# Kernel tuning notes

Hardware: AMD Instinct MI355X
Metric: run time of the kernel (lower is better)

## Reference

```python
import jax, jax.numpy as jnp
import numpy as np

EPS = 1e-5


def conv2d(x, w, b=None, stride=1, padding=0, dilation=1, groups=1):
    out = jax.lax.conv_general_dilated(
        x, w, (stride, stride), [(padding, padding), (padding, padding)],
        rhs_dilation=(dilation, dilation),
        dimension_numbers=('NCHW', 'OIHW', 'NCHW'),
        feature_group_count=groups)
    if b is not None:
        out = out + b[None, :, None, None]
    return out


def unfold3(x):
    # torch nn.Unfold(kernel=3, padding=1), kept as [b, c, 9, h, w]
    # (channel-major ordering c*9+k, k = row-major kernel index, matches torch)
    b, c, h, w = x.shape
    xp = jnp.pad(x, ((0, 0), (0, 0), (1, 1), (1, 1)))
    return jnp.stack([xp[:, :, i:i + h, j:j + w]
                      for i in range(3) for j in range(3)], axis=2)


def setup_inputs():
    B, C, O, H, W = 8, 64, 64, 128, 128
    key = jax.random.key(0)
    ks = jax.random.split(key, 16)
    s = 0.05
    rn = lambda k, shape: jax.random.normal(k, shape, jnp.float32) * s
    return {
        'x': jax.random.normal(ks[0], (B, C, H, W), jnp.float32),
        'cdcm_conv1_w': rn(ks[1], (C, C, 1, 1)),
        'cdcm_conv1_b': jnp.zeros((C,), jnp.float32),
        'cdcm_w5': rn(ks[2], (C, C, 3, 3)),
        'cdcm_w7': rn(ks[3], (C, C, 3, 3)),
        'cdcm_w9': rn(ks[4], (C, C, 3, 3)),
        'cdcm_w11': rn(ks[5], (C, C, 3, 3)),
        'dsc_dw_w': rn(ks[6], (C, 1, 3, 3)),
        'dsc_dw_b': jnp.zeros((C,), jnp.float32),
        'dsc_pw_w': rn(ks[7], (C, C, 1, 1)),
        'dsc_pw_b': jnp.zeros((C,), jnp.float32),
        'gw_w': rn(ks[8], (C, 9, 9)),
        'gw_b': jnp.zeros((C, 9), jnp.float32),
        'gw_bn_g': jnp.ones((C, 9), jnp.float32),
        'gw_bn_b': jnp.zeros((C, 9), jnp.float32),
        'gw_bn_m': jnp.zeros((C, 9), jnp.float32),
        'gw_bn_v': jnp.ones((C, 9), jnp.float32),
        'conv_w': rn(ks[9], (O, C, 3, 3)),
        'conv_b': jnp.zeros((O,), jnp.float32),
        'fr_w': rn(ks[10], (O, O, 1, 1)),
        'fr_b': jnp.zeros((O,), jnp.float32),
        'ens_w': rn(ks[11], (3, O, O, 3, 3)),
        'ens_b': jnp.zeros((3, O), jnp.float32),
        'bn_g': jnp.ones((O,), jnp.float32),
        'bn_b': jnp.zeros((O,), jnp.float32),
        'bn_m': jnp.zeros((O,), jnp.float32),
        'bn_v': jnp.ones((O,), jnp.float32),
    }


def reference(x, cdcm_conv1_w, cdcm_conv1_b, cdcm_w5, cdcm_w7, cdcm_w9, cdcm_w11,
              dsc_dw_w, dsc_dw_b, dsc_pw_w, dsc_pw_b,
              gw_w, gw_b, gw_bn_g, gw_bn_b, gw_bn_m, gw_bn_v,
              conv_w, conv_b, fr_w, fr_b, ens_w, ens_b,
              bn_g, bn_b, bn_m, bn_v):
    C = x.shape[1]
    # ---- CDCM: relu -> 1x1 conv -> 4 dilated 3x3 convs, each through the
    # SAME DepthwiseSeparableConv instance, then summed ----
    y = conv2d(jax.nn.relu(x), cdcm_conv1_w, cdcm_conv1_b)

    def dsc(z):
        z = conv2d(z, dsc_dw_w, dsc_dw_b, padding=1, groups=C)
        return conv2d(z, dsc_pw_w, dsc_pw_b)

    y = sum(dsc(conv2d(y, w, padding=d, dilation=d))
            for w, d in ((cdcm_w5, 5), (cdcm_w7, 7), (cdcm_w9, 9), (cdcm_w11, 11)))

    b, c, h, w = y.shape
    patches = unfold3(y)  # [b, c, 9, h, w]

    # ---- dynamic weight generation: grouped 1x1 conv (groups=c, 9->9 per
    # group) + inference BatchNorm over the c*9 channels + softmax over the 9
    # patch positions ----
    gw = jnp.einsum('coi,bcihw->bcohw', gw_w, patches) + gw_b[None, :, :, None, None]
    scale = (gw_bn_g / jnp.sqrt(gw_bn_v + EPS))[None, :, :, None, None]
    gw = (gw - gw_bn_m[None, :, :, None, None]) * scale + gw_bn_b[None, :, :, None, None]
    wsm = jax.nn.softmax(gw, axis=2)

    # ---- involution core: the rearrange to (3h,3w) + stride-3 3x3 conv is
    # exactly a contraction of (patches * weights) with the conv kernel over
    # the 9 kernel positions (row-major kernel index == patch index) ----
    prod = patches * wsm  # [b, c, 9, h, w]
    O = conv_w.shape[0]
    out = jnp.einsum('bckhw,ock->bohw', prod, conv_w.reshape(O, c, 9)) + conv_b[None, :, None, None]

    # ---- feature reuse: conv1x1(conv_out) + conv_out ----
    out = conv2d(out, fr_w, fr_b) + out

    # ---- ensemble: mean of 3 conv3x3 ----
    out = jnp.mean(jnp.stack([conv2d(out, ens_w[i], ens_b[i], padding=1)
                              for i in range(3)]), axis=0)

    # ---- final BN (inference) + ReLU ----
    out = (out - bn_m[None, :, None, None]) * (bn_g / jnp.sqrt(bn_v + EPS))[None, :, None, None] \
          + bn_b[None, :, None, None]
    return jax.nn.relu(out)
```

## Files before the change

### kernel.cpp

```cpp
#include <hip/hip_runtime.h>
#include <hip/hip_bf16.h>
#include <hip/hip_fp16.h>

#define EPSV 1e-5f
#define Bn 8
#define Cn 64
#define Hn 128
#define Wn 128
#define Pn (Hn*Wn)
#define PR 150
#define PE 130
#define YPAD_ELEMS (Bn*PR*PR*Cn)

typedef _Float16 v8h __attribute__((ext_vector_type(8)));
typedef float v16f __attribute__((ext_vector_type(16)));
typedef unsigned short ushort8v __attribute__((ext_vector_type(8)));
typedef unsigned short ushort4v __attribute__((ext_vector_type(4)));

__device__ __forceinline__ unsigned short f2h(float v) {
  _Float16 h = (_Float16)v;
  return *reinterpret_cast<const unsigned short*>(&h);
}

__device__ __forceinline__ v8h exp8h(v8h x) {
  union { v8h v; __half2 h[4]; } u; u.v = x;
  #pragma unroll
  for (int i = 0; i < 4; i++) u.h[i] = h2exp(u.h[i]);
  return u.v;
}
__device__ __forceinline__ v8h rcp8h(v8h x) {
  union { v8h v; __half2 h[4]; } u; u.v = x;
  #pragma unroll
  for (int i = 0; i < 4; i++) u.h[i] = h2rcp(u.h[i]);
  return u.v;
}

__device__ __forceinline__ size_t clb(int b, int row, int kb, int col, int PD) {
  return ((((size_t)b * PD + row) * 4 + kb) * PD + col) * 16;
}

__device__ __forceinline__ void swz_bh(int& b, int& h) {
  int bid = blockIdx.x;
  int w = (bid & 7) * 128 + (bid >> 3);
  b = w >> 7; h = w & 127;
}

__global__ __launch_bounds__(256) void k_prep(
    const float* __restrict__ w1, const float* __restrict__ w5,
    const float* __restrict__ w7, const float* __restrict__ w9,
    const float* __restrict__ w11, const float* __restrict__ pww,
    const float* __restrict__ frw, const float* __restrict__ cw,
    const float* __restrict__ gww, const float* __restrict__ gwb,
    const float* __restrict__ gbg, const float* __restrict__ gbb,
    const float* __restrict__ gbm, const float* __restrict__ gbv,
    const float* __restrict__ ensw, const float* __restrict__ ensb,
    const float* __restrict__ bng, const float* __restrict__ bnb,
    const float* __restrict__ bnm, const float* __restrict__ bnv,
    unsigned short* __restrict__ apack, unsigned short* __restrict__ apinv,
    unsigned short* __restrict__ apens, unsigned short* __restrict__ appw1,
    unsigned short* __restrict__ appw, unsigned short* __restrict__ apfr,
    unsigned short* __restrict__ apid, unsigned short* __restrict__ gwpk,
    unsigned short* __restrict__ apk, unsigned short* __restrict__ bpk,
    float* __restrict__ esc, float* __restrict__ ebi)
{
  int id = blockIdx.x * 256 + threadIdx.x;
  if (id < 147456) {
    int e = id & 7, l = (id >> 3) & 63, mh = (id >> 9) & 1,
        kb = (id >> 10) & 3, tap = id >> 12;
    int d = tap / 9, k9 = tap - 9 * d;
    int m = mh * 32 + (l & 31);
    int c = kb * 16 + (l >> 5) * 8 + e;
    const float* src = (d == 0) ? w5 : (d == 1) ? w7 : (d == 2) ? w9 : w11;
    apack[id] = f2h(src[(m * 64 + c) * 9 + k9]);
    return;
  }
  id -= 147456;
  if (id < 36864) {
    int e = id & 7, l = (id >> 3) & 63, mh = (id >> 9) & 1,
        kb = (id >> 10) & 3, tap = id >> 12;
    int m = mh * 32 + (l & 31);
    int c = kb * 16 + (l >> 5) * 8 + e;
    apinv[id] = f2h(cw[(m * 64 + c) * 9 + tap]);
    return;
  }
  id -= 36864;
  if (id < 36864) {
    int e = id & 7, l = (id >> 3) & 63, mh = (id >> 9) & 1,
        kb = (id >> 10) & 3, tap = id >> 12;
    int m = mh * 32 + (l & 31);
    int c = kb * 16 + (l >> 5) * 8 + e;
    float v = (ensw[((0 * 64 + m) * 64 + c) * 9 + tap] +
               ensw[((64 + m) * 64 + c) * 9 + tap] +
               ensw[((128 + m) * 64 + c) * 9 + tap]) * (1.f / 3.f);
    apens[id] = f2h(v);
    return;
  }
  id -= 36864;
  if (id < 4096) {
    int e = id & 7, l = (id >> 3) & 63, mh = (id >> 9) & 1, kb = (id >> 10) & 3;
    int m = mh * 32 + (l & 31);
    int c = kb * 16 + (l >> 5) * 8 + e;
    appw1[id] = f2h(w1[m * 64 + c]);
    return;
  }
  id -= 4096;
  if (id < 4096) {
    int e = id & 7, l = (id >> 3) & 63, mh = (id >> 9) & 1, kb = (id >> 10) & 3;
    int m = mh * 32 + (l & 31);
    int c = kb * 16 + (l >> 5) * 8 + e;
    appw[id] = f2h(pww[m * 64 + c]);
    return;
  }
  id -= 4096;
  if (id < 4096) {
    int e = id & 7, l = (id >> 3) & 63, mh = (id >> 9) & 1, kb = (id >> 10) & 3;
    int m = mh * 32 + (l & 31);
    int c = kb * 16 + (l >> 5) * 8 + e;
    apfr[id] = f2h(frw[m * 64 + c]);
    return;
  }
  id -= 4096;
  if (id < 4096) {
    int e = id & 7, l = (id >> 3) & 63, mh = (id >> 9) & 1, kb = (id >> 10) & 3;
    int m = mh * 32 + (l & 31);
    int c = kb * 16 + (l >> 5) * 8 + e;
    apid[id] = f2h((m == c) ? 1.f : 0.f);
    return;
  }
  id -= 4096;
  if (id < 5184) {
    int cblk = id / 648, r = id - cblk * 648;
    int tap = r >> 3, ch = r & 7;
    int c = cblk * 8 + ch;
    gwpk[id] = f2h(gww[c * 81 + tap]);
    return;
  }
  id -= 5184;
  if (id < 576) {
    int cblk = id / 72, r = id - cblk * 72;
    int o = r >> 3, ch = r & 7;
    int c = cblk * 8 + ch;
    float A = gbg[c * 9 + o] / sqrtf(gbv[c * 9 + o] + EPSV);
    apk[id] = f2h(A);
    return;
  }
  id -= 576;
  if (id < 576) {
    int cblk = id / 72, r = id - cblk * 72;
    int o = r >> 3, ch = r & 7;
    int c = cblk * 8 + ch;
    float A = gbg[c * 9 + o] / sqrtf(gbv[c * 9 + o] + EPSV);
    float B = (gwb[c * 9 + o] - gbm[c * 9 + o]) * A + gbb[c * 9 + o];
    bpk[id] = f2h(B);
    return;
  }
  id -= 576;
  if (id < 64) {
    float s = bng[id] / sqrtf(bnv[id] + EPSV);
    esc[id] = s;
    float bm = (ensb[id] + ensb[64 + id] + ensb[128 + id]) * (1.f / 3.f);
    ebi[id] = (bm - bnm[id]) * s + bnb[id];
  }
}

__global__ __launch_bounds__(256) void k_zb(unsigned short* __restrict__ buf,
                                            int PD, int pad)
{
  int per_b = 2 * pad * PD + 128 * 2 * pad;
  int id = blockIdx.x * 256 + threadIdx.x;
  int b = id / per_b;
  if (b >= Bn) return;
  int r = id - b * per_b;
  int tb = 2 * pad * PD;
  int row, col;
  if (r < tb) {
    int rr = r / PD; col = r - rr * PD;
    row = (rr < pad) ? rr : (rr + 128);
  } else {
    int r2 = r - tb;
    row = pad + r2 / (2 * pad);
    int cc = r2 - (r2 / (2 * pad)) * (2 * pad);
    col = (cc < pad) ? cc : (cc + 128);
  }
  ushort8v z = {0, 0, 0, 0, 0, 0, 0, 0};
  #pragma unroll
  for (int kb = 0; kb < 4; kb++) {
    unsigned short* p = buf + clb(b, row, kb, col, PD);
    *(ushort8v*)p = z;
    *(ushort8v*)(p + 8) = z;
  }
}

__global__ __launch_bounds__(256, 4) void k_pw1x(const float* __restrict__ x,
    const unsigned short* __restrict__ apw, const float* __restrict__ bias,
    unsigned short* __restrict__ ypad)
{
  int b, h; swz_bh(b, h);
  const int tid = threadIdx.x, wv = tid >> 6, l = tid & 63;
  const int ln31 = l & 31, g = l >> 5;
  const int px = wv * 32 + ln31;
  const float* xb = x + ((size_t)b * Cn) * Pn + h * Wn + px;
  v16f acc0, acc1;
  #pragma unroll
  for (int r = 0; r < 16; r++) { acc0[r] = 0.f; acc1[r] = 0.f; }
  const unsigned short* apl = apw + l * 8;
  #pragma unroll
  for (int kb = 0; kb < 4; kb++) {
    int c0 = kb * 16 + g * 8;
    v8h Bf;
    #pragma unroll
    for (int e = 0; e < 8; e++)
      Bf[e] = (_Float16)fmaxf(xb[(size_t)(c0 + e) * Pn], 0.f);
    v8h A0 = *(const v8h*)(apl + (kb * 2) * 512);
    v8h A1 = *(const v8h*)(apl + (kb * 2 + 1) * 512);
    acc0 = __builtin_amdgcn_mfma_f32_32x32x16_f16(A0, Bf, acc0, 0, 0, 0);
    acc1 = __builtin_amdgcn_mfma_f32_32x32x16_f16(A1, Bf, acc1, 0, 0, 0);
  }
  #pragma unroll
  for (int t = 0; t < 4; t++) {
    int c0 = 8 * t + 4 * g;
    int kb = c0 >> 4, sub = c0 & 15;
    ushort4v s0, s1;
    #pragma unroll
    for (int u = 0; u < 4; u++) {
      s0[u] = f2h(acc0[4 * t + u] + bias[c0 + u]);
      s1[u] = f2h(acc1[4 * t + u] + bias[c0 + u + 32]);
    }
    *(ushort4v*)(ypad + clb(b, h + 11, kb, px + 11, PR) + sub) = s0;
    *(ushort4v*)(ypad + clb(b, h + 11, kb + 2, px + 11, PR) + sub) = s1;
  }
}

__global__ __launch_bounds__(256) void k_cdcm_mfma(
    const unsigned short* __restrict__ ypad,
    const unsigned short* __restrict__ apack,
    unsigned short* __restrict__ spad)
{
  __shared__ __align__(16) unsigned short Abuf[36864];
  int b, h; swz_bh(b, h);
  const int tid = threadIdx.x, wv = tid >> 6, l = tid & 63;
  const int ln31 = l & 31, g = l >> 5;

  v16f acc0, acc1;
  #pragma unroll
  for (int r = 0; r < 16; r++) { acc0[r] = 0.f; acc1[r] = 0.f; }

  const unsigned short* abl = Abuf + l * 8;

  for (int d = 0; d < 4; d++) {
    __syncthreads();
    {
      const ushort8v* src = (const ushort8v*)(apack + d * 36864);
      ushort8v* dst = (ushort8v*)Abuf;
      #pragma unroll
      for (int it = 0; it < 18; it++)
        dst[tid + it * 256] = src[tid + it * 256];
    }
    __syncthreads();

    const int dil = 5 + 2 * d;
    #pragma unroll
    for (int ky = 0; ky < 3; ky++) {
      const int row = h + 11 + (ky - 1) * dil;
      #pragma unroll
      for (int kx = 0; kx < 3; kx++) {
        const int col = wv * 32 + ln31 + (kx - 1) * dil + 11;
        const int t9 = ky * 3 + kx;
        const unsigned short* ap = abl + t9 * 4096;
        #pragma unroll
        for (int kb = 0; kb < 4; kb++) {
          v8h Bf = *(const v8h*)(ypad + clb(b, row, kb, col, PR) + g * 8);
          v8h A0 = *(const v8h*)(ap + kb * 1024);
          v8h A1 = *(const v8h*)(ap + kb * 1024 + 512);
          acc0 = __builtin_amdgcn_mfma_f32_32x32x16_f16(A0, Bf, acc0, 0, 0, 0);
          acc1 = __builtin_amdgcn_mfma_f32_32x32x16_f16(A1, Bf, acc1, 0, 0, 0);
        }
      }
    }
  }
  const int px = wv * 32 + ln31;
  #pragma unroll
  for (int t = 0; t < 4; t++) {
    int c0 = 8 * t + 4 * g;
    int kb = c0 >> 4, sub = c0 & 15;
    ushort4v s0, s1;
    #pragma unroll
    for (int u = 0; u < 4; u++) {
      s0[u] = f2h(acc0[4 * t + u]);
      s1[u] = f2h(acc1[4 * t + u]);
    }
    *(ushort4v*)(spad + clb(b, h + 1, kb, px + 1, PE) + sub) = s0;
    *(ushort4v*)(spad + clb(b, h + 1, kb + 2, px + 1, PE) + sub) = s1;
  }
}

__global__ __launch_bounds__(256, 4) void k_dwpw_mfma(
    const unsigned short* __restrict__ spad,
    const float* __restrict__ dww, const float* __restrict__ dwb,
    const unsigned short* __restrict__ appw, const float* __restrict__ pwb,
    unsigned short* __restrict__ y2pad)
{
  __shared__ float wdw[576];
  __shared__ float bdw[64];
  const int tid = threadIdx.x;
  for (int t = tid; t < 576; t += 256) wdw[t] = dww[t];
  if (tid < 64) bdw[tid] = dwb[tid];
  __syncthreads();

  int b, h; swz_bh(b, h);
  const int wv = tid >> 6, l = tid & 63;
  const int ln31 = l & 31, g = l >> 5;
  const int w = wv * 32 + ln31;

  v16f acc0, acc1;
  #pragma unroll
  for (int r = 0; r < 16; r++) { acc0[r] = 0.f; acc1[r] = 0.f; }
  const unsigned short* apl = appw + l * 8;

  #pragma unroll
  for (int kb = 0; kb < 4; kb++) {
    const int c0 = kb * 16 + g * 8;
    v8h t[9];
    #pragma unroll
    for (int k = 0; k < 9; k++) {
      const int dy = k / 3 - 1, dx = k % 3 - 1;
      t[k] = *(const v8h*)(spad + clb(b, h + 1 + dy, kb, w + 1 + dx, PE) + g * 8);
    }
    v8h dvh;
    #pragma unroll
    for (int e = 0; e < 8; e++) {
      const int c = c0 + e;
      float a = 4.f * bdw[c];
      #pragma unroll
      for (int k = 0; k < 9; k++) a += wdw[c * 9 + k] * (float)t[k][e];
      dvh[e] = (_Float16)a;
    }
    v8h A0 = *(const v8h*)(apl + (kb * 2) * 512);
    v8h A1 = *(const v8h*)(apl + (kb * 2 + 1) * 512);
    acc0 = __builtin_amdgcn_mfma_f32_32x32x16_f16(A0, dvh, acc0, 0, 0, 0);
    acc1 = __builtin_amdgcn_mfma_f32_32x32x16_f16(A1, dvh, acc1, 0, 0, 0);
  }
  #pragma unroll
  for (int t = 0; t < 4; t++) {
    int c0 = 8 * t + 4 * g;
    int kb = c0 >> 4, sub = c0 & 15;
    ushort4v s0, s1;
    #pragma unroll
    for (int u = 0; u < 4; u++) {
      s0[u] = f2h(acc0[4 * t + u] + 4.f * pwb[c0 + u]);
      s1[u] = f2h(acc1[4 * t + u] + 4.f * pwb[c0 + u + 32]);
    }
    *(ushort4v*)(y2pad + clb(b, h + 1, kb, w + 1, PE) + sub) = s0;
    *(ushort4v*)(y2pad + clb(b, h + 1, kb + 2, w + 1, PE) + sub) = s1;
  }
}

__global__ __launch_bounds__(256, 3) void k_invol_mfma(
    const unsigned short* __restrict__ y2pad,
    const unsigned short* __restrict__ gwpk,
    const unsigned short* __restrict__ apk,
    const unsigned short* __restrict__ bpk,
    const unsigned short* __restrict__ apinv,
    const float* __restrict__ cbias,
    unsigned short* __restrict__ ipad)
{
  __shared__ __align__(16) unsigned short gws[5184];
  __shared__ __align__(16) unsigned short As[576];
  __shared__ __align__(16) unsigned short Bs[576];
  const int tid = threadIdx.x;
  for (int t = tid; t < 648; t += 256)
    ((ushort8v*)gws)[t] = ((const ushort8v*)gwpk)[t];
  if (tid < 72) {
    ((ushort8v*)As)[tid] = ((const ushort8v*)apk)[tid];
    ((ushort8v*)Bs)[tid] = ((const ushort8v*)bpk)[tid];
  }
  __syncthreads();

  int b, h; swz_bh(b, h);
  const int wv = tid >> 6, l = tid & 63;
  const int p32 = l & 31, g = l >> 5;
  const int w = wv * 32 + p32;

  v16f acc0, acc1;
  #pragma unroll
  for (int r = 0; r < 16; r++) { acc0[r] = 0.f; acc1[r] = 0.f; }

  for (int cb4 = 0; cb4 < 4; cb4++) {
    const int cblk = cb4 * 2 + g;
    const unsigned short* gwp = gws + cblk * 648;
    const unsigned short* Ap = As + cblk * 72;
    const unsigned short* Bp = Bs + cblk * 72;

    v8h pt[9];
    #pragma unroll
    for (int k = 0; k < 9; k++) {
      const int dy = k / 3 - 1, dx = k % 3 - 1;
      pt[k] = *(const v8h*)(y2pad + clb(b, h + 1 + dy, cb4, w + 1 + dx, PE) + g * 8);
    }
    v8h s[9];
    #pragma unroll
    for (int o = 0; o < 9; o++) {
      v8h a = (*(const v8h*)(gwp + o * 72)) * pt[0];
      #pragma unroll
      for (int i = 1; i < 9; i++)
        a += (*(const v8h*)(gwp + o * 72 + i * 8)) * pt[i];
      s[o] = a * (*(const v8h*)(Ap + o * 8)) + (*(const v8h*)(Bp + o * 8));
    }
    v8h esum = {0, 0, 0, 0, 0, 0, 0, 0};
    #pragma unroll
    for (int o = 0; o < 9; o++) { s[o] = exp8h(s[o]); esum += s[o]; }
    v8h inv = rcp8h(esum);
    #pragma unroll
    for (int k = 0; k < 9; k++) pt[k] = pt[k] * s[k] * inv;

    const unsigned short* ap = apinv + l * 8;
    #pragma unroll
    for (int k = 0; k < 9; k++) {
      const unsigned short* a2 = ap + ((k * 4 + cb4) * 2) * 512;
      v8h A0 = *(const v8h*)(a2);
      v8h A1 = *(const v8h*)(a2 + 512);
      acc0 = __builtin_amdgcn_mfma_f32_32x32x16_f16(A0, pt[k], acc0, 0, 0, 0);
      acc1 = __builtin_amdgcn_mfma_f32_32x32x16_f16(A1, pt[k], acc1, 0, 0, 0);
    }
  }
  #pragma unroll
  for (int t = 0; t < 4; t++) {
    int c0 = 8 * t + 4 * g;
    int kb = c0 >> 4, sub = c0 & 15;
    ushort4v s0, s1;
    #pragma unroll
    for (int u = 0; u < 4; u++) {
      s0[u] = f2h(acc0[4 * t + u] + cbias[c0 + u]);
      s1[u] = f2h(acc1[4 * t + u] + cbias[c0 + u + 32]);
    }
    *(ushort4v*)(ipad + clb(b, h, kb, w, 128) + sub) = s0;
    *(ushort4v*)(ipad + clb(b, h, kb + 2, w, 128) + sub) = s1;
  }
}

__global__ __launch_bounds__(256, 4) void k_fr_mfma(
    const unsigned short* __restrict__ ipad,
    const unsigned short* __restrict__ apfr,
    const unsigned short* __restrict__ apid,
    const float* __restrict__ bias,
    unsigned short* __restrict__ opad)
{
  int b, h; swz_bh(b, h);
  const int tid = threadIdx.x, wv = tid >> 6, l = tid & 63;
  const int ln31 = l & 31, g = l >> 5;
  const int px = wv * 32 + ln31;
  v16f acc0, acc1;
  #pragma unroll
  for (int r = 0; r < 16; r++) { acc0[r] = 0.f; acc1[r] = 0.f; }
  const unsigned short* apl = apfr + l * 8;
  const unsigned short* idl = apid + l * 8;
  #pragma unroll
  for (int kb = 0; kb < 4; kb++) {
    v8h Bf = *(const v8h*)(ipad + clb(b, h, kb, px, 128) + g * 8);
    v8h A0 = *(const v8h*)(apl + (kb * 2) * 512);
    v8h A1 = *(const v8h*)(apl + (kb * 2 + 1) * 512);
    v8h I0 = *(const v8h*)(idl + (kb * 2) * 512);
    v8h I1 = *(const v8h*)(idl + (kb * 2 + 1) * 512);
    acc0 = __builtin_amdgcn_mfma_f32_32x32x16_f16(A0, Bf, acc0, 0, 0, 0);
    acc1 = __builtin_amdgcn_mfma_f32_32x32x16_f16(A1, Bf, acc1, 0, 0, 0);
    acc0 = __builtin_amdgcn_mfma_f32_32x32x16_f16(I0, Bf, acc0, 0, 0, 0);
    acc1 = __builtin_amdgcn_mfma_f32_32x32x16_f16(I1, Bf, acc1, 0, 0, 0);
  }
  #pragma unroll
  for (int t = 0; t < 4; t++) {
    int c0 = 8 * t + 4 * g;
    int kb = c0 >> 4, sub = c0 & 15;
    ushort4v s0, s1;
    #pragma unroll
    for (int u = 0; u < 4; u++) {
      s0[u] = f2h(acc0[4 * t + u] + bias[c0 + u]);
      s1[u] = f2h(acc1[4 * t + u] + bias[c0 + u + 32]);
    }
    *(ushort4v*)(opad + clb(b, h + 1, kb, px + 1, PE) + sub) = s0;
    *(ushort4v*)(opad + clb(b, h + 1, kb + 2, px + 1, PE) + sub) = s1;
  }
}

__global__ __launch_bounds__(256) void k_ens_mfma(
    const unsigned short* __restrict__ opad,
    const unsigned short* __restrict__ apens,
    const float* __restrict__ esc, const float* __restrict__ ebi,
    float* __restrict__ out)
{
  __shared__ __align__(16) unsigned short Abuf[36864];
  const int tid = threadIdx.x;
  {
    const ushort8v* src = (const ushort8v*)apens;
    ushort8v* dst = (ushort8v*)Abuf;
    #pragma unroll
    for (int it = 0; it < 18; it++)
      dst[tid + it * 256] = src[tid + it * 256];
  }
  __syncthreads();

  int b, h; swz_bh(b, h);
  const int wv = tid >> 6, l = tid & 63;
  const int ln31 = l & 31, g = l >> 5;

  v16f acc0, acc1;
  #pragma unroll
  for (int r = 0; r < 16; r++) { acc0[r] = 0.f; acc1[r] = 0.f; }

  const unsigned short* abl = Abuf + l * 8;

  #pragma unroll
  for (int ky = 0; ky < 3; ky++) {
    #pragma unroll
    for (int kx = 0; kx < 3; kx++) {
      const int tap = ky * 3 + kx;
      const int row = h + ky;
      const int col = wv * 32 + ln31 + kx;
      const unsigned short* ap = abl + tap * 4096;
      #pragma unroll
      for (int kb = 0; kb < 4; kb++) {
        v8h Bf = *(const v8h*)(opad + clb(b, row, kb, col, PE) + g * 8);
        v8h A0 = *(const v8h*)(ap + kb * 1024);
        v8h A1 = *(const v8h*)(ap + kb * 1024 + 512);
        acc0 = __builtin_amdgcn_mfma_f32_32x32x16_f16(A0, Bf, acc0, 0, 0, 0);
        acc1 = __builtin_amdgcn_mfma_f32_32x32x16_f16(A1, Bf, acc1, 0, 0, 0);
      }
    }
  }
  float* sp = out + ((size_t)b * Cn) * Pn + h * Wn + wv * 32 + ln31;
  #pragma unroll
  for (int r = 0; r < 16; r++) {
    int o0 = (r & 3) + 8 * (r >> 2) + 4 * g;
    float v0 = acc0[r] * esc[o0] + ebi[o0];
    float v1 = acc1[r] * esc[o0 + 32] + ebi[o0 + 32];
    sp[(size_t)o0 * Pn] = fmaxf(v0, 0.f);
    sp[(size_t)(o0 + 32) * Pn] = fmaxf(v1, 0.f);
  }
}

extern "C" void kernel_launch(void* const* d_in, const int* in_sizes, int n_in,
                              void* d_out, int out_size, void* d_ws, size_t ws_size,
                              hipStream_t stream)
{
  const float* x    = (const float*)d_in[0];
  const float* w1   = (const float*)d_in[1];
  const float* b1   = (const float*)d_in[2];
  const float* w5   = (const float*)d_in[3];
  const float* w7   = (const float*)d_in[4];
  const float* w9   = (const float*)d_in[5];
  const float* w11  = (const float*)d_in[6];
  const float* dww  = (const float*)d_in[7];
  const float* dwb  = (const float*)d_in[8];
  const float* pww  = (const float*)d_in[9];
  const float* pwb  = (const float*)d_in[10];
  const float* gww  = (const float*)d_in[11];
  const float* gwb  = (const float*)d_in[12];
  const float* gbg  = (const float*)d_in[13];
  const float* gbb  = (const float*)d_in[14];
  const float* gbm  = (const float*)d_in[15];
  const float* gbv  = (const float*)d_in[16];
  const float* cw   = (const float*)d_in[17];
  const float* cb   = (const float*)d_in[18];
  const float* frw  = (const float*)d_in[19];
  const float* frb  = (const float*)d_in[20];
  const float* ensw = (const float*)d_in[21];
  const float* ensb = (const float*)d_in[22];
  const float* bng  = (const float*)d_in[23];
  const float* bnb  = (const float*)d_in[24];
  const float* bnm  = (const float*)d_in[25];
  const float* bnv  = (const float*)d_in[26];

  unsigned short* wsu   = (unsigned short*)d_ws;
  unsigned short* ypad  = wsu;
  unsigned short* y2pad = wsu;
  unsigned short* opad  = wsu;
  unsigned short* apack = wsu + YPAD_ELEMS;
  unsigned short* apinv = apack + 147456;
  unsigned short* apens = apinv + 36864;
  unsigned short* appw1 = apens + 36864;
  unsigned short* appw  = appw1 + 4096;
  unsigned short* apfr  = appw + 4096;
  unsigned short* apid  = apfr + 4096;
  unsigned short* gwpk  = apid + 4096;
  unsigned short* apk   = gwpk + 5184;
  unsigned short* bpk   = apk + 576;
  float* esc = (float*)(bpk + 576);
  float* ebi = esc + 64;

  unsigned short* spad = (unsigned short*)d_out;
  unsigned short* ipad = (unsigned short*)d_out;
  float* D = (float*)d_out;

  k_prep<<<953, 256, 0, stream>>>(w1, w5, w7, w9, w11, pww, frw, cw,
                                  gww, gwb, gbg, gbb, gbm, gbv, ensw, ensb,
                                  bng, bnb, bnm, bnv,
                                  apack, apinv, apens, appw1, appw, apfr, apid,
                                  gwpk, apk, bpk, esc, ebi);
  k_zb<<<192, 256, 0, stream>>>(ypad, PR, 11);
  k_zb<<<17, 256, 0, stream>>>(spad, PE, 1);

  k_pw1x<<<1024, 256, 0, stream>>>(x, appw1, b1, ypad);
  k_cdcm_mfma<<<1024, 256, 0, stream>>>(ypad, apack, spad);
  k_zb<<<17, 256, 0, stream>>>(y2pad, PE, 1);
  k_dwpw_mfma<<<1024, 256, 0, stream>>>(spad, dww, dwb, appw, pwb, y2pad);
  k_invol_mfma<<<1024, 256, 0, stream>>>(y2pad, gwpk, apk, bpk, apinv, cb, ipad);
  k_fr_mfma<<<1024, 256, 0, stream>>>(ipad, apfr, apid, frb, opad);
  k_ens_mfma<<<1024, 256, 0, stream>>>(opad, apens, esc, ebi, D);
}
```

Before: 166.5 us.

## Compute two output rows per block in dilated and ensemble convs; drop identity MFMA

The CDCM and ensemble conv kernels now give each block two output rows, with four accumulators. Each LDS-staged A fragment is reused across both rows and the grid is halved, which cuts the LDS weight reload per row. The feature-reuse kernel stops adding the residual through an identity-matrix MFMA and instead reads the fp16 input and adds it in the epilogue, so the identity weight pack is removed. The costs are higher register pressure from four v16f accumulators, fewer blocks, and the loss of the block-to-(b,h) swizzle.

```diff
diff --git a/kernel.cpp b/kernel.cpp
--- a/kernel.cpp
+++ b/kernel.cpp
@@ -20,6 +20,9 @@
 __device__ __forceinline__ unsigned short f2h(float v) {
   _Float16 h = (_Float16)v;
   return *reinterpret_cast<const unsigned short*>(&h);
+}
+__device__ __forceinline__ float h2f(unsigned short u) {
+  return (float)(*reinterpret_cast<const _Float16*>(&u));
 }
 
 __device__ __forceinline__ v8h exp8h(v8h x) {
@@ -59,7 +62,7 @@
     unsigned short* __restrict__ apack, unsigned short* __restrict__ apinv,
     unsigned short* __restrict__ apens, unsigned short* __restrict__ appw1,
     unsigned short* __restrict__ appw, unsigned short* __restrict__ apfr,
-    unsigned short* __restrict__ apid, unsigned short* __restrict__ gwpk,
+    unsigned short* __restrict__ gwpk,
     unsigned short* __restrict__ apk, unsigned short* __restrict__ bpk,
     float* __restrict__ esc, float* __restrict__ ebi)
 {
@@ -117,14 +120,6 @@
     int m = mh * 32 + (l & 31);
     int c = kb * 16 + (l >> 5) * 8 + e;
     apfr[id] = f2h(frw[m * 64 + c]);
-    return;
-  }
-  id -= 4096;
-  if (id < 4096) {
-    int e = id & 7, l = (id >> 3) & 63, mh = (id >> 9) & 1, kb = (id >> 10) & 3;
-    int m = mh * 32 + (l & 31);
-    int c = kb * 16 + (l >> 5) * 8 + e;
-    apid[id] = f2h((m == c) ? 1.f : 0.f);
     return;
   }
   id -= 4096;
@@ -237,13 +232,14 @@
     unsigned short* __restrict__ spad)
 {
   __shared__ __align__(16) unsigned short Abuf[36864];
-  int b, h; swz_bh(b, h);
+  const int bid = blockIdx.x;
+  const int b = bid & 7, h0 = (bid >> 3) * 2;
   const int tid = threadIdx.x, wv = tid >> 6, l = tid & 63;
   const int ln31 = l & 31, g = l >> 5;
 
-  v16f acc0, acc1;
-  #pragma unroll
-  for (int r = 0; r < 16; r++) { acc0[r] = 0.f; acc1[r] = 0.f; }
+  v16f a00, a01, a10, a11;
+  #pragma unroll
+  for (int r = 0; r < 16; r++) { a00[r] = 0.f; a01[r] = 0.f; a10[r] = 0.f; a11[r] = 0.f; }
 
   const unsigned short* abl = Abuf + l * 8;
 
@@ -261,7 +257,7 @@
     const int dil = 5 + 2 * d;
     #pragma unroll
     for (int ky = 0; ky < 3; ky++) {
-      const int row = h + 11 + (ky - 1) * dil;
+      const int r0 = h0 + 11 + (ky - 1) * dil;
       #pragma unroll
       for (int kx = 0; kx < 3; kx++) {
         const int col = wv * 32 + ln31 + (kx - 1) * dil + 11;
@@ -269,11 +265,14 @@
         const unsigned short* ap = abl + t9 * 4096;
         #pragma unroll
         for (int kb = 0; kb < 4; kb++) {
-          v8h Bf = *(const v8h*)(ypad + clb(b, row, kb, col, PR) + g * 8);
+          v8h B0 = *(const v8h*)(ypad + clb(b, r0, kb, col, PR) + g * 8);
+          v8h B1 = *(const v8h*)(ypad + clb(b, r0 + 1, kb, col, PR) + g * 8);
           v8h A0 = *(const v8h*)(ap + kb * 1024);
           v8h A1 = *(const v8h*)(ap + kb * 1024 + 512);
-          acc0 = __builtin_amdgcn_mfma_f32_32x32x16_f16(A0, Bf, acc0, 0, 0, 0);
-          acc1 = __builtin_amdgcn_mfma_f32_32x32x16_f16(A1, Bf, acc1, 0, 0, 0);
+          a00 = __builtin_amdgcn_mfma_f32_32x32x16_f16(A0, B0, a00, 0, 0, 0);
+          a01 = __builtin_amdgcn_mfma_f32_32x32x16_f16(A1, B0, a01, 0, 0, 0);
+          a10 = __builtin_amdgcn_mfma_f32_32x32x16_f16(A0, B1, a10, 0, 0, 0);
+          a11 = __builtin_amdgcn_mfma_f32_32x32x16_f16(A1, B1, a11, 0, 0, 0);
         }
       }
     }
@@ -283,14 +282,18 @@
   for (int t = 0; t < 4; t++) {
     int c0 = 8 * t + 4 * g;
     int kb = c0 >> 4, sub = c0 & 15;
-    ushort4v s0, s1;
+    ushort4v s0, s1, s2, s3;
     #pragma unroll
     for (int u = 0; u < 4; u++) {
-      s0[u] = f2h(acc0[4 * t + u]);
-      s1[u] = f2h(acc1[4 * t + u]);
-    }
-    *(ushort4v*)(spad + clb(b, h + 1, kb, px + 1, PE) + sub) = s0;
-    *(ushort4v*)(spad + clb(b, h + 1, kb + 2, px + 1, PE) + sub) = s1;
+      s0[u] = f2h(a00[4 * t + u]);
+      s1[u] = f2h(a01[4 * t + u]);
+      s2[u] = f2h(a10[4 * t + u]);
+      s3[u] = f2h(a11[4 * t + u]);
+    }
+    *(ushort4v*)(spad + clb(b, h0 + 1, kb, px + 1, PE) + sub) = s0;
+    *(ushort4v*)(spad + clb(b, h0 + 1, kb + 2, px + 1, PE) + sub) = s1;
+    *(ushort4v*)(spad + clb(b, h0 + 2, kb, px + 1, PE) + sub) = s2;
+    *(ushort4v*)(spad + clb(b, h0 + 2, kb + 2, px + 1, PE) + sub) = s3;
   }
 }
 
@@ -441,7 +444,6 @@
 __global__ __launch_bounds__(256, 4) void k_fr_mfma(
     const unsigned short* __restrict__ ipad,
     const unsigned short* __restrict__ apfr,
-    const unsigned short* __restrict__ apid,
     const float* __restrict__ bias,
     unsigned short* __restrict__ opad)
 {
@@ -453,28 +455,25 @@
   #pragma unroll
   for (int r = 0; r < 16; r++) { acc0[r] = 0.f; acc1[r] = 0.f; }
   const unsigned short* apl = apfr + l * 8;
-  const unsigned short* idl = apid + l * 8;
   #pragma unroll
   for (int kb = 0; kb < 4; kb++) {
     v8h Bf = *(const v8h*)(ipad + clb(b, h, kb, px, 128) + g * 8);
     v8h A0 = *(const v8h*)(apl + (kb * 2) * 512);
     v8h A1 = *(const v8h*)(apl + (kb * 2 + 1) * 512);
-    v8h I0 = *(const v8h*)(idl + (kb * 2) * 512);
-    v8h I1 = *(const v8h*)(idl + (kb * 2 + 1) * 512);
     acc0 = __builtin_amdgcn_mfma_f32_32x32x16_f16(A0, Bf, acc0, 0, 0, 0);
     acc1 = __builtin_amdgcn_mfma_f32_32x32x16_f16(A1, Bf, acc1, 0, 0, 0);
-    acc0 = __builtin_amdgcn_mfma_f32_32x32x16_f16(I0, Bf, acc0, 0, 0, 0);
-    acc1 = __builtin_amdgcn_mfma_f32_32x32x16_f16(I1, Bf, acc1, 0, 0, 0);
   }
   #pragma unroll
   for (int t = 0; t < 4; t++) {
     int c0 = 8 * t + 4 * g;
     int kb = c0 >> 4, sub = c0 & 15;
+    ushort4v r0 = *(const ushort4v*)(ipad + clb(b, h, kb, px, 128) + sub);
+    ushort4v r1 = *(const ushort4v*)(ipad + clb(b, h, kb + 2, px, 128) + sub);
     ushort4v s0, s1;
     #pragma unroll
     for (int u = 0; u < 4; u++) {
-      s0[u] = f2h(acc0[4 * t + u] + bias[c0 + u]);
-      s1[u] = f2h(acc1[4 * t + u] + bias[c0 + u + 32]);
+      s0[u] = f2h(acc0[4 * t + u] + bias[c0 + u] + h2f(r0[u]));
+      s1[u] = f2h(acc1[4 * t + u] + bias[c0 + u + 32] + h2f(r1[u]));
     }
     *(ushort4v*)(opad + clb(b, h + 1, kb, px + 1, PE) + sub) = s0;
     *(ushort4v*)(opad + clb(b, h + 1, kb + 2, px + 1, PE) + sub) = s1;
@@ -498,13 +497,14 @@
   }
   __syncthreads();
 
-  int b, h; swz_bh(b, h);
+  const int bid = blockIdx.x;
+  const int b = bid & 7, h0 = (bid >> 3) * 2;
   const int wv = tid >> 6, l = tid & 63;
   const int ln31 = l & 31, g = l >> 5;
 
-  v16f acc0, acc1;
-  #pragma unroll
-  for (int r = 0; r < 16; r++) { acc0[r] = 0.f; acc1[r] = 0.f; }
+  v16f a00, a01, a10, a11;
+  #pragma unroll
+  for (int r = 0; r < 16; r++) { a00[r] = 0.f; a01[r] = 0.f; a10[r] = 0.f; a11[r] = 0.f; }
 
   const unsigned short* abl = Abuf + l * 8;
 
@@ -513,27 +513,33 @@
     #pragma unroll
     for (int kx = 0; kx < 3; kx++) {
       const int tap = ky * 3 + kx;
-      const int row = h + ky;
+      const int r0 = h0 + ky;
       const int col = wv * 32 + ln31 + kx;
       const unsigned short* ap = abl + tap * 4096;
       #pragma unroll
       for (int kb = 0; kb < 4; kb++) {
-        v8h Bf = *(const v8h*)(opad + clb(b, row, kb, col, PE) + g * 8);
+        v8h B0 = *(const v8h*)(opad + clb(b, r0, kb, col, PE) + g * 8);
+        v8h B1 = *(const v8h*)(opad + clb(b, r0 + 1, kb, col, PE) + g * 8);
         v8h A0 = *(const v8h*)(ap + kb * 1024);
         v8h A1 = *(const v8h*)(ap + kb * 1024 + 512);
-        acc0 = __builtin_amdgcn_mfma_f32_32x32x16_f16(A0, Bf, acc0, 0, 0, 0);
-        acc1 = __builtin_amdgcn_mfma_f32_32x32x16_f16(A1, Bf, acc1, 0, 0, 0);
+        a00 = __builtin_amdgcn_mfma_f32_32x32x16_f16(A0, B0, a00, 0, 0, 0);
+        a01 = __builtin_amdgcn_mfma_f32_32x32x16_f16(A1, B0, a01, 0, 0, 0);
+        a10 = __builtin_amdgcn_mfma_f32_32x32x16_f16(A0, B1, a10, 0, 0, 0);
+        a11 = __builtin_amdgcn_mfma_f32_32x32x16_f16(A1, B1, a11, 0, 0, 0);
       }
     }
   }
-  float* sp = out + ((size_t)b * Cn) * Pn + h * Wn + wv * 32 + ln31;
+  float* sp0 = out + ((size_t)b * Cn) * Pn + h0 * Wn + wv * 32 + ln31;
+  float* sp1 = sp0 + Wn;
   #pragma unroll
   for (int r = 0; r < 16; r++) {
     int o0 = (r & 3) + 8 * (r >> 2) + 4 * g;
-    float v0 = acc0[r] * esc[o0] + ebi[o0];
-    float v1 = acc1[r] * esc[o0 + 32] + ebi[o0 + 32];
-    sp[(size_t)o0 * Pn] = fmaxf(v0, 0.f);
-    sp[(size_t)(o0 + 32) * Pn] = fmaxf(v1, 0.f);
+    float e0 = esc[o0], e1 = esc[o0 + 32];
+    float i0 = ebi[o0], i1 = ebi[o0 + 32];
+    sp0[(size_t)o0 * Pn] = fmaxf(a00[r] * e0 + i0, 0.f);
+    sp0[(size_t)(o0 + 32) * Pn] = fmaxf(a01[r] * e1 + i1, 0.f);
+    sp1[(size_t)o0 * Pn] = fmaxf(a10[r] * e0 + i0, 0.f);
+    sp1[(size_t)(o0 + 32) * Pn] = fmaxf(a11[r] * e1 + i1, 0.f);
   }
 }
 
@@ -579,8 +585,7 @@
   unsigned short* appw1 = apens + 36864;
   unsigned short* appw  = appw1 + 4096;
   unsigned short* apfr  = appw + 4096;
-  unsigned short* apid  = apfr + 4096;
-  unsigned short* gwpk  = apid + 4096;
+  unsigned short* gwpk  = apfr + 4096;
   unsigned short* apk   = gwpk + 5184;
   unsigned short* bpk   = apk + 576;
   float* esc = (float*)(bpk + 576);
@@ -590,19 +595,19 @@
   unsigned short* ipad = (unsigned short*)d_out;
   float* D = (float*)d_out;
 
-  k_prep<<<953, 256, 0, stream>>>(w1, w5, w7, w9, w11, pww, frw, cw,
+  k_prep<<<937, 256, 0, stream>>>(w1, w5, w7, w9, w11, pww, frw, cw,
                                   gww, gwb, gbg, gbb, gbm, gbv, ensw, ensb,
                                   bng, bnb, bnm, bnv,
-                                  apack, apinv, apens, appw1, appw, apfr, apid,
+                                  apack, apinv, apens, appw1, appw, apfr,
                                   gwpk, apk, bpk, esc, ebi);
   k_zb<<<192, 256, 0, stream>>>(ypad, PR, 11);
   k_zb<<<17, 256, 0, stream>>>(spad, PE, 1);
 
   k_pw1x<<<1024, 256, 0, stream>>>(x, appw1, b1, ypad);
-  k_cdcm_mfma<<<1024, 256, 0, stream>>>(ypad, apack, spad);
+  k_cdcm_mfma<<<512, 256, 0, stream>>>(ypad, apack, spad);
   k_zb<<<17, 256, 0, stream>>>(y2pad, PE, 1);
   k_dwpw_mfma<<<1024, 256, 0, stream>>>(spad, dww, dwb, appw, pwb, y2pad);
   k_invol_mfma<<<1024, 256, 0, stream>>>(y2pad, gwpk, apk, bpk, apinv, cb, ipad);
-  k_fr_mfma<<<1024, 256, 0, stream>>>(ipad, apfr, apid, frb, opad);
-  k_ens_mfma<<<1024, 256, 0, stream>>>(opad, apens, esc, ebi, D);
-}
+  k_fr_mfma<<<1024, 256, 0, stream>>>(ipad, apfr, frb, opad);
+  k_ens_mfma<<<512, 256, 0, stream>>>(opad, apens, esc, ebi, D);
+}
```

After: 164.7 us. No clear change (-1.1%).
